# Performance work log

Hardware: AMD Instinct MI355X
Metric: run time of the kernel (lower is better)

## Reference

```python
import jax, jax.numpy as jnp
import numpy as np

B, S, D, MAXOBJ = 512, 77, 2048, 4
EPS = 1e-5


def _layer_norm(x, g, b):
    mu = jnp.mean(x, axis=-1, keepdims=True)
    var = jnp.mean((x - mu) ** 2, axis=-1, keepdims=True)
    return (x - mu) / jnp.sqrt(var + EPS) * g + b


def _mlp(x, ln_g, ln_b, w1, b1, w2, b2, residual):
    h = _layer_norm(x, ln_g, ln_b)
    h = jax.nn.gelu(h @ w1 + b1, approximate=False)
    h = h @ w2 + b2
    return h + x if residual else h


def setup_inputs() -> dict:
    key = jax.random.key(0)
    ks = jax.random.split(key, 8)
    sc = 0.02
    inputs_embeds = jax.random.normal(ks[0], (B, S, D), dtype=jnp.float32)
    # exactly one image token per sample -> mask sum matches fused rows
    pos = jax.random.randint(ks[1], (B,), 0, S)
    image_token_mask = (jnp.arange(S)[None, :] == pos[:, None])  # bool [B,S]
    object_embeds = jax.random.normal(ks[2], (B, MAXOBJ, 1, D), dtype=jnp.float32)
    num_objects = jax.random.randint(ks[3], (B,), 1, MAXOBJ + 1)  # >=1 objects
    return {
        "inputs_embeds": inputs_embeds,
        "object_embeds": object_embeds,
        "mlp1_ln_g": jnp.ones((2 * D,), jnp.float32),
        "mlp1_ln_b": jnp.zeros((2 * D,), jnp.float32),
        "mlp1_w1": sc * jax.random.normal(ks[4], (2 * D, D), jnp.float32),
        "mlp1_b1": jnp.zeros((D,), jnp.float32),
        "mlp1_w2": sc * jax.random.normal(ks[5], (D, D), jnp.float32),
        "mlp1_b2": jnp.zeros((D,), jnp.float32),
        "mlp2_ln_g": jnp.ones((D,), jnp.float32),
        "mlp2_ln_b": jnp.zeros((D,), jnp.float32),
        "mlp2_w1": sc * jax.random.normal(ks[6], (D, D), jnp.float32),
        "mlp2_b1": jnp.zeros((D,), jnp.float32),
        "mlp2_w2": sc * jax.random.normal(ks[7], (D, D), jnp.float32),
        "mlp2_b2": jnp.zeros((D,), jnp.float32),
        "ln_g": jnp.ones((D,), jnp.float32),
        "ln_b": jnp.zeros((D,), jnp.float32),
        "image_token_mask": image_token_mask,
        "num_objects": num_objects,
    }


def reference(inputs_embeds, object_embeds,
              mlp1_ln_g, mlp1_ln_b, mlp1_w1, mlp1_b1, mlp1_w2, mlp1_b2,
              mlp2_ln_g, mlp2_ln_b, mlp2_w1, mlp2_b1, mlp2_w2, mlp2_b2,
              ln_g, ln_b, image_token_mask, num_objects):
    b, s, d = inputs_embeds.shape
    max_obj = object_embeds.shape[1]
    dt = inputs_embeds.dtype
    # mean over valid objects per sample (fuse_object_embeddings ragged split+mean)
    valid = (jnp.arange(max_obj)[None, :] < num_objects[:, None]).astype(dt)  # [B,MAXOBJ]
    obj = object_embeds[:, :, 0, :]  # [B,MAXOBJ,D] (T==1 token per object)
    mean_obj = jnp.sum(obj * valid[:, :, None], axis=1) / num_objects[:, None].astype(dt)
    # gather the single image-token embed per row (mask has exactly one True per row)
    idx = jnp.argmax(image_token_mask, axis=1)  # [B]
    rows = jnp.arange(b)
    tok = inputs_embeds[rows, idx]  # [B,D]
    # fuse_fn: cat -> MLP1 (no residual) + tok -> MLP2 (residual) -> LayerNorm
    x = jnp.concatenate([tok, mean_obj], axis=-1)  # [B,2D]
    h = _mlp(x, mlp1_ln_g, mlp1_ln_b, mlp1_w1, mlp1_b1, mlp1_w2, mlp1_b2, residual=False) + tok
    h = _mlp(h, mlp2_ln_g, mlp2_ln_b, mlp2_w1, mlp2_b1, mlp2_w2, mlp2_b2, residual=True)
    h = _layer_norm(h, ln_g, ln_b)
    # masked_scatter_ back into the sequence
    out = inputs_embeds.at[rows, idx].set(h.astype(dt))
    return out
```

## Files before the change

kernel.cpp:

```cpp
#include <hip/hip_runtime.h>
#include <math.h>

#define B_ 512
#define S_ 77
#define D_ 2048
#define EPS_ 1e-5f

typedef __attribute__((ext_vector_type(8))) short bf16x8;
typedef __attribute__((ext_vector_type(4))) float f32x4;

__device__ __forceinline__ unsigned short f2bf(float f) {
  union { float f; unsigned u; } x; x.f = f;
  return (unsigned short)((x.u + 0x7FFFu + ((x.u >> 16) & 1u)) >> 16);
}

__device__ __forceinline__ void blockReduce2(float& a, float& b, float* sbuf) {
  #pragma unroll
  for (int off = 32; off > 0; off >>= 1) {
    a += __shfl_down(a, off, 64);
    b += __shfl_down(b, off, 64);
  }
  int lane = threadIdx.x & 63, wid = threadIdx.x >> 6;
  if (lane == 0) { sbuf[wid * 2] = a; sbuf[wid * 2 + 1] = b; }
  __syncthreads();
  if (threadIdx.x == 0) {
    float sa = 0.f, sb = 0.f;
    #pragma unroll
    for (int w = 0; w < 4; w++) { sa += sbuf[w * 2]; sb += sbuf[w * 2 + 1]; }
    sbuf[8] = sa; sbuf[9] = sb;
  }
  __syncthreads();
  a = sbuf[8]; b = sbuf[9];
}

__global__ __launch_bounds__(256)
void prep_wcvt_kernel(const float* __restrict__ w1, const float* __restrict__ w2,
                      const float* __restrict__ w3, const float* __restrict__ w4,
                      unsigned short* __restrict__ o1, unsigned short* __restrict__ o2,
                      unsigned short* __restrict__ o3, unsigned short* __restrict__ o4,
                      const float* __restrict__ x_embed, const float* __restrict__ obj,
                      const int* __restrict__ mask, const int* __restrict__ nobj,
                      const float* __restrict__ g, const float* __restrict__ bb,
                      int* __restrict__ idx_out, float* __restrict__ tok_out,
                      unsigned short* __restrict__ xln_out) {
  __shared__ unsigned short T[64 * 72];
  __shared__ int s_idx;
  __shared__ float sbuf[10];
  const int z = blockIdx.z;
  const int t = threadIdx.x;

  if (z == 4) {
    const int b = blockIdx.y * gridDim.x + blockIdx.x;
    if (b >= B_) return;
    if (t == 0) s_idx = 0;
    __syncthreads();
    for (int j = t; j < S_; j += 256)
      if (mask[b * S_ + j] != 0) atomicMax(&s_idx, j);
    __syncthreads();
    const int idx = s_idx;
    if (t == 0) idx_out[b] = idx;

    const float4* tokrow = (const float4*)(x_embed + ((long)b * S_ + idx) * D_);
    float4 t0 = tokrow[t * 2];
    float4 t1 = tokrow[t * 2 + 1];
    ((float4*)(tok_out + (long)b * D_))[t * 2] = t0;
    ((float4*)(tok_out + (long)b * D_))[t * 2 + 1] = t1;

    const int n = nobj[b];
    const float inv_n = 1.0f / (float)n;
    float4 s0 = make_float4(0.f, 0.f, 0.f, 0.f), s1 = s0;
    for (int o = 0; o < n; o++) {
      const float4* orow = (const float4*)(obj + ((long)b * 4 + o) * D_);
      float4 q0 = orow[t * 2], q1 = orow[t * 2 + 1];
      s0.x += q0.x; s0.y += q0.y; s0.z += q0.z; s0.w += q0.w;
      s1.x += q1.x; s1.y += q1.y; s1.z += q1.z; s1.w += q1.w;
    }
    float vals[16] = { t0.x, t0.y, t0.z, t0.w, t1.x, t1.y, t1.z, t1.w,
                       s0.x * inv_n, s0.y * inv_n, s0.z * inv_n, s0.w * inv_n,
                       s1.x * inv_n, s1.y * inv_n, s1.z * inv_n, s1.w * inv_n };
    float sum = 0.f, sq = 0.f;
    #pragma unroll
    for (int i = 0; i < 16; i++) { sum += vals[i]; sq += vals[i] * vals[i]; }
    blockReduce2(sum, sq, sbuf);
    const float mu = sum * (1.f / 4096.f);
    const float rstd = rsqrtf(sq * (1.f / 4096.f) - mu * mu + EPS_);
    #pragma unroll
    for (int i = 0; i < 16; i++) {
      int d = (i < 8) ? (t * 8 + i) : (D_ + t * 8 + (i - 8));
      float v = (vals[i] - mu) * rstd * g[d] + bb[d];
      xln_out[(long)b * (2 * D_) + d] = f2bf(v);
    }
    return;
  }

  const int K = (z == 0) ? 4096 : 2048;
  if ((int)blockIdx.y * 64 >= K) return;
  const float* W = (z == 0) ? w1 : (z == 1) ? w2 : (z == 2) ? w3 : w4;
  unsigned short* O = (z == 0) ? o1 : (z == 1) ? o2 : (z == 2) ? o3 : o4;
  const int k0 = blockIdx.y * 64, n0 = blockIdx.x * 64;
  const int r = t >> 4, c4 = (t & 15) * 4;
  #pragma unroll
  for (int rr = 0; rr < 4; rr++) {
    const int k = rr * 16 + r;
    float4 v = *(const float4*)&W[(long)(k0 + k) * 2048 + n0 + c4];
    T[(c4 + 0) * 72 + k] = f2bf(v.x);
    T[(c4 + 1) * 72 + k] = f2bf(v.y);
    T[(c4 + 2) * 72 + k] = f2bf(v.z);
    T[(c4 + 3) * 72 + k] = f2bf(v.w);
  }
  __syncthreads();
  const int n = t >> 3, k8 = (t & 7) * 8;
  *(uint4*)&O[(long)(n0 + n) * K + k0 + k8]      = *(const uint4*)&T[n * 72 + k8];
  *(uint4*)&O[(long)(n0 + n + 32) * K + k0 + k8] = *(const uint4*)&T[(n + 32) * 72 + k8];
}

template<int GELU, int HAS_RES, int OUT_BF16>
__global__ __launch_bounds__(256)
void gemm_kernel(const unsigned short* __restrict__ A, const unsigned short* __restrict__ Wt,
                 const float* __restrict__ bias, const float* __restrict__ res,
                 void* __restrict__ outp, int M, int N, int K,
                 const float4* __restrict__ csrc, float4* __restrict__ cdst, long cn4) {
  const int mblocks = M >> 6;
  if ((int)blockIdx.y >= mblocks) {
    const int cby = gridDim.y - mblocks;
    const long tcount = (long)cby * gridDim.x * blockDim.x;
    long i = ((long)((int)blockIdx.y - mblocks) * gridDim.x + blockIdx.x) * blockDim.x + threadIdx.x;
    const long lim = cn4 - 3 * tcount;
    for (; i < lim; i += 4 * tcount) {
      float4 v0 = csrc[i];
      float4 v1 = csrc[i + tcount];
      float4 v2 = csrc[i + 2 * tcount];
      float4 v3 = csrc[i + 3 * tcount];
      cdst[i] = v0;
      cdst[i + tcount] = v1;
      cdst[i + 2 * tcount] = v2;
      cdst[i + 3 * tcount] = v3;
    }
    for (; i < cn4; i += tcount) cdst[i] = csrc[i];
    return;
  }
  constexpr int LDA = 72;
  __shared__ __align__(16) unsigned short As[2][64 * LDA];
  __shared__ __align__(16) unsigned short Bs[2][64 * LDA];
  const int tid = threadIdx.x;
  const int m0 = blockIdx.y * 64;
  const int n0 = blockIdx.x * 64;
  const int lane = tid & 63;
  const int wave = tid >> 6;
  const int l16 = lane & 15;
  const int quad = lane >> 4;
  const int wm = (wave & 1) * 32;
  const int wn = (wave >> 1) * 32;
  const int srow = tid >> 3;
  const int scol = (tid & 7) * 8;

  const unsigned short* Ar0 = A  + (long)(m0 + srow) * K + scol;
  const unsigned short* Ar1 = A  + (long)(m0 + srow + 32) * K + scol;
  const unsigned short* Br0 = Wt + (long)(n0 + srow) * K + scol;
  const unsigned short* Br1 = Wt + (long)(n0 + srow + 32) * K + scol;

  f32x4 acc[2][2];
  #pragma unroll
  for (int i = 0; i < 2; i++)
    #pragma unroll
    for (int j = 0; j < 2; j++) acc[i][j] = (f32x4){0.f, 0.f, 0.f, 0.f};

  const int ntile = K >> 6;

  uint4 ra0 = *(const uint4*)Ar0, ra1 = *(const uint4*)Ar1;
  uint4 rb0 = *(const uint4*)Br0, rb1 = *(const uint4*)Br1;
  *(uint4*)&As[0][srow * LDA + scol]        = ra0;
  *(uint4*)&As[0][(srow + 32) * LDA + scol] = ra1;
  *(uint4*)&Bs[0][srow * LDA + scol]        = rb0;
  *(uint4*)&Bs[0][(srow + 32) * LDA + scol] = rb1;
  if (ntile > 1) {
    ra0 = *(const uint4*)(Ar0 + 64); ra1 = *(const uint4*)(Ar1 + 64);
    rb0 = *(const uint4*)(Br0 + 64); rb1 = *(const uint4*)(Br1 + 64);
  }
  __syncthreads();

  for (int t = 0; t < ntile; ++t) {
    const unsigned short* as = As[t & 1];
    const unsigned short* bs = Bs[t & 1];
    bf16x8 af[2][2], bg[2][2];
    #pragma unroll
    for (int kk = 0; kk < 2; kk++) {
      af[kk][0] = *(const bf16x8*)&as[(wm + l16) * LDA + kk * 32 + quad * 8];
      af[kk][1] = *(const bf16x8*)&as[(wm + 16 + l16) * LDA + kk * 32 + quad * 8];
      bg[kk][0] = *(const bf16x8*)&bs[(wn + l16) * LDA + kk * 32 + quad * 8];
      bg[kk][1] = *(const bf16x8*)&bs[(wn + 16 + l16) * LDA + kk * 32 + quad * 8];
    }
    if (t + 1 < ntile) {
      unsigned short* an = As[(t + 1) & 1];
      unsigned short* bn = Bs[(t + 1) & 1];
      *(uint4*)&an[srow * LDA + scol]        = ra0;
      *(uint4*)&an[(srow + 32) * LDA + scol] = ra1;
      *(uint4*)&bn[srow * LDA + scol]        = rb0;
      *(uint4*)&bn[(srow + 32) * LDA + scol] = rb1;
      if (t + 2 < ntile) {
        const int off = (t + 2) << 6;
        ra0 = *(const uint4*)(Ar0 + off); ra1 = *(const uint4*)(Ar1 + off);
        rb0 = *(const uint4*)(Br0 + off); rb1 = *(const uint4*)(Br1 + off);
      }
    }
    #pragma unroll
    for (int kk = 0; kk < 2; kk++)
      #pragma unroll
      for (int mt = 0; mt < 2; mt++)
        #pragma unroll
        for (int nt2 = 0; nt2 < 2; nt2++)
          acc[mt][nt2] = __builtin_amdgcn_mfma_f32_16x16x32_bf16(af[kk][mt], bg[kk][nt2], acc[mt][nt2], 0, 0, 0);
    __syncthreads();
  }
  #pragma unroll
  for (int mt = 0; mt < 2; mt++) {
    #pragma unroll
    for (int nt2 = 0; nt2 < 2; nt2++) {
      const int col = n0 + wn + nt2 * 16 + l16;
      const float bc = bias[col];
      #pragma unroll
      for (int r = 0; r < 4; r++) {
        const int row = m0 + wm + mt * 16 + quad * 4 + r;
        float v = acc[mt][nt2][r] + bc;
        if constexpr (HAS_RES) v += res[(long)row * N + col];
        if constexpr (GELU) v = 0.5f * v * (1.f + erff(v * 0.70710678118654752f));
        if constexpr (OUT_BF16)
          ((unsigned short*)outp)[(long)row * N + col] = f2bf(v);
        else
          ((float*)outp)[(long)row * N + col] = v;
      }
    }
  }
}

__global__ __launch_bounds__(256)
void ln_bf16_kernel(const float* __restrict__ in, const float* __restrict__ g,
                    const float* __restrict__ bb, unsigned short* __restrict__ out) {
  __shared__ float sbuf[10];
  const int b = blockIdx.x, t = threadIdx.x;
  const float4* row = (const float4*)(in + (long)b * D_);
  float4 v0 = row[t * 2], v1 = row[t * 2 + 1];
  float o[8] = { v0.x, v0.y, v0.z, v0.w, v1.x, v1.y, v1.z, v1.w };
  float sum = 0.f, sq = 0.f;
  #pragma unroll
  for (int i = 0; i < 8; i++) { sum += o[i]; sq += o[i] * o[i]; }
  blockReduce2(sum, sq, sbuf);
  const float mu = sum * (1.f / 2048.f);
  const float rstd = rsqrtf(sq * (1.f / 2048.f) - mu * mu + EPS_);
  const int d0 = t * 8;
  #pragma unroll
  for (int i = 0; i < 8; i++)
    out[(long)b * D_ + d0 + i] = f2bf((o[i] - mu) * rstd * g[d0 + i] + bb[d0 + i]);
}

__global__ __launch_bounds__(256)
void final_kernel(const float* __restrict__ in, const float* __restrict__ g,
                  const float* __restrict__ bb, const int* __restrict__ idxbuf,
                  float* __restrict__ out) {
  __shared__ float sbuf[10];
  const int b = blockIdx.x, t = threadIdx.x;
  const float4* row = (const float4*)(in + (long)b * D_);
  float4 v0 = row[t * 2], v1 = row[t * 2 + 1];
  float o[8] = { v0.x, v0.y, v0.z, v0.w, v1.x, v1.y, v1.z, v1.w };
  float sum = 0.f, sq = 0.f;
  #pragma unroll
  for (int i = 0; i < 8; i++) { sum += o[i]; sq += o[i] * o[i]; }
  blockReduce2(sum, sq, sbuf);
  const float mu = sum * (1.f / 2048.f);
  const float rstd = rsqrtf(sq * (1.f / 2048.f) - mu * mu + EPS_);
  float* orow = out + ((long)b * S_ + idxbuf[b]) * D_;
  const int d0 = t * 8;
  #pragma unroll
  for (int i = 0; i < 8; i++) o[i] = (o[i] - mu) * rstd * g[d0 + i] + bb[d0 + i];
  ((float4*)orow)[t * 2]     = make_float4(o[0], o[1], o[2], o[3]);
  ((float4*)orow)[t * 2 + 1] = make_float4(o[4], o[5], o[6], o[7]);
}

extern "C" void kernel_launch(void* const* d_in, const int* in_sizes, int n_in,
                              void* d_out, int out_size, void* d_ws, size_t ws_size,
                              hipStream_t stream) {
  const float* inputs_embeds = (const float*)d_in[0];
  const float* object_embeds = (const float*)d_in[1];
  const float* mlp1_ln_g = (const float*)d_in[2];
  const float* mlp1_ln_b = (const float*)d_in[3];
  const float* mlp1_w1   = (const float*)d_in[4];
  const float* mlp1_b1   = (const float*)d_in[5];
  const float* mlp1_w2   = (const float*)d_in[6];
  const float* mlp1_b2   = (const float*)d_in[7];
  const float* mlp2_ln_g = (const float*)d_in[8];
  const float* mlp2_ln_b = (const float*)d_in[9];
  const float* mlp2_w1   = (const float*)d_in[10];
  const float* mlp2_b1   = (const float*)d_in[11];
  const float* mlp2_w2   = (const float*)d_in[12];
  const float* mlp2_b2   = (const float*)d_in[13];
  const float* ln_g      = (const float*)d_in[14];
  const float* ln_b      = (const float*)d_in[15];
  const int* mask        = (const int*)d_in[16];
  const int* nobj        = (const int*)d_in[17];

  char* ws = (char*)d_ws;
  int*            idxbuf = (int*)ws;
  float*          tok    = (float*)(ws + 4096);
  unsigned short* xln    = (unsigned short*)(ws + 4096 + 4194304);
  unsigned short* h1     = (unsigned short*)(ws + 4096 + 8388608);
  float*          h2     = (float*)(ws + 4096 + 10485760);
  unsigned short* x2ln   = (unsigned short*)(ws + 4096 + 14680064);
  unsigned short* h3     = (unsigned short*)(ws + 4096 + 16777216);
  float*          h4     = (float*)(ws + 4096 + 18874368);
  char*           wbase  = ws + 4096 + 18874368 + 4194304;
  unsigned short* w1t    = (unsigned short*)(wbase);
  unsigned short* w2t    = (unsigned short*)(wbase + 16777216);
  unsigned short* w3t    = (unsigned short*)(wbase + 25165824);
  unsigned short* w4t    = (unsigned short*)(wbase + 33554432);

  prep_wcvt_kernel<<<dim3(32, 64, 5), 256, 0, stream>>>(
      mlp1_w1, mlp1_w2, mlp2_w1, mlp2_w2, w1t, w2t, w3t, w4t,
      inputs_embeds, object_embeds, mask, nobj, mlp1_ln_g, mlp1_ln_b,
      idxbuf, tok, xln);

  const float4* in4 = (const float4*)inputs_embeds;
  float4* out4 = (float4*)d_out;
  const long n4 = (long)B_ * S_ * D_ / 4;
  const long ch = n4 / 4;

  dim3 gg(2048 / 64, B_ / 64 + 16);
  gemm_kernel<1, 0, 1><<<gg, 256, 0, stream>>>(xln,  w1t, mlp1_b1, nullptr, h1, B_, D_, 2 * D_,
                                               in4 + 0 * ch, out4 + 0 * ch, ch);
  gemm_kernel<0, 1, 0><<<gg, 256, 0, stream>>>(h1,   w2t, mlp1_b2, tok,     h2, B_, D_, D_,
                                               in4 + 1 * ch, out4 + 1 * ch, ch);
  ln_bf16_kernel<<<B_, 256, 0, stream>>>(h2, mlp2_ln_g, mlp2_ln_b, x2ln);
  gemm_kernel<1, 0, 1><<<gg, 256, 0, stream>>>(x2ln, w3t, mlp2_b1, nullptr, h3, B_, D_, D_,
                                               in4 + 2 * ch, out4 + 2 * ch, ch);
  gemm_kernel<0, 1, 0><<<gg, 256, 0, stream>>>(h3,   w4t, mlp2_b2, h2,      h4, B_, D_, D_,
                                               in4 + 3 * ch, out4 + 3 * ch, ch);
  final_kernel<<<B_, 256, 0, stream>>>(h4, ln_g, ln_b, idxbuf, (float*)d_out);
}
```

Baseline: 680.9 us.

## Move embed copy into prep kernel and deepen GEMM global-load prefetch to four stages

The full inputs_embeds to output copy no longer rides in extra blocks of each of the four GEMM launches. It now runs as a sixth z-slice of the weight-conversion/prep kernel, so the GEMMs launch only their compute tiles. The GEMM main loop is unrolled by four with register staging that issues global loads four K-tiles ahead, while keeping double-buffered LDS. This hides more memory latency but raises register pressure, and the copy now competes with weight conversion instead of overlapping the GEMMs.

```diff
diff --git a/kernel.cpp b/kernel.cpp
--- a/kernel.cpp
+++ b/kernel.cpp
@@ -34,20 +34,38 @@
 }
 
 __global__ __launch_bounds__(256)
-void prep_wcvt_kernel(const float* __restrict__ w1, const float* __restrict__ w2,
-                      const float* __restrict__ w3, const float* __restrict__ w4,
-                      unsigned short* __restrict__ o1, unsigned short* __restrict__ o2,
-                      unsigned short* __restrict__ o3, unsigned short* __restrict__ o4,
-                      const float* __restrict__ x_embed, const float* __restrict__ obj,
-                      const int* __restrict__ mask, const int* __restrict__ nobj,
-                      const float* __restrict__ g, const float* __restrict__ bb,
-                      int* __restrict__ idx_out, float* __restrict__ tok_out,
-                      unsigned short* __restrict__ xln_out) {
+void mega_stream_kernel(const float* __restrict__ w1, const float* __restrict__ w2,
+                        const float* __restrict__ w3, const float* __restrict__ w4,
+                        unsigned short* __restrict__ o1, unsigned short* __restrict__ o2,
+                        unsigned short* __restrict__ o3, unsigned short* __restrict__ o4,
+                        const float* __restrict__ x_embed, const float* __restrict__ obj,
+                        const int* __restrict__ mask, const int* __restrict__ nobj,
+                        const float* __restrict__ g, const float* __restrict__ bb,
+                        int* __restrict__ idx_out, float* __restrict__ tok_out,
+                        unsigned short* __restrict__ xln_out,
+                        const float4* __restrict__ csrc, float4* __restrict__ cdst, long cn4) {
   __shared__ unsigned short T[64 * 72];
   __shared__ int s_idx;
   __shared__ float sbuf[10];
   const int z = blockIdx.z;
   const int t = threadIdx.x;
+
+  if (z == 5) {
+    const long tcount = (long)2048 * 256;
+    long i = ((long)blockIdx.y * gridDim.x + blockIdx.x) * 256 + t;
+    for (; i + 3 * tcount < cn4; i += 4 * tcount) {
+      float4 v0 = csrc[i];
+      float4 v1 = csrc[i + tcount];
+      float4 v2 = csrc[i + 2 * tcount];
+      float4 v3 = csrc[i + 3 * tcount];
+      cdst[i] = v0;
+      cdst[i + tcount] = v1;
+      cdst[i + 2 * tcount] = v2;
+      cdst[i + 3 * tcount] = v3;
+    }
+    for (; i < cn4; i += tcount) cdst[i] = csrc[i];
+    return;
+  }
 
   if (z == 4) {
     const int b = blockIdx.y * gridDim.x + blockIdx.x;
@@ -114,31 +132,46 @@
   *(uint4*)&O[(long)(n0 + n + 32) * K + k0 + k8] = *(const uint4*)&T[(n + 32) * 72 + k8];
 }
 
+
+#define DECL_STAGE(s) uint4 sa0_##s, sa1_##s, sb0_##s, sb1_##s;
+#define LOAD_STAGE(s, tt) { const long off_ = (long)(tt) << 6; \
+  sa0_##s = *(const uint4*)(Ar0 + off_); sa1_##s = *(const uint4*)(Ar1 + off_); \
+  sb0_##s = *(const uint4*)(Br0 + off_); sb1_##s = *(const uint4*)(Br1 + off_); }
+#define WRITE_STAGE(s, buf) { \
+  *(uint4*)&As[buf][srow * LDA + scol]        = sa0_##s; \
+  *(uint4*)&As[buf][(srow + 32) * LDA + scol] = sa1_##s; \
+  *(uint4*)&Bs[buf][srow * LDA + scol]        = sb0_##s; \
+  *(uint4*)&Bs[buf][(srow + 32) * LDA + scol] = sb1_##s; }
+
+#define GEMM_STEP(c, snext, curbuf, nextbuf) { \
+  const int t_ = tb + (c); \
+  if (t_ + 4 < ntile) LOAD_STAGE(c, t_ + 4) \
+  const unsigned short* as_ = As[curbuf]; \
+  const unsigned short* bs_ = Bs[curbuf]; \
+  bf16x8 af[2][2], bg[2][2]; \
+  _Pragma("unroll") \
+  for (int kk = 0; kk < 2; kk++) { \
+    af[kk][0] = *(const bf16x8*)&as_[(wm + l16) * LDA + kk * 32 + quad * 8]; \
+    af[kk][1] = *(const bf16x8*)&as_[(wm + 16 + l16) * LDA + kk * 32 + quad * 8]; \
+    bg[kk][0] = *(const bf16x8*)&bs_[(wn + l16) * LDA + kk * 32 + quad * 8]; \
+    bg[kk][1] = *(const bf16x8*)&bs_[(wn + 16 + l16) * LDA + kk * 32 + quad * 8]; \
+  } \
+  _Pragma("unroll") \
+  for (int kk = 0; kk < 2; kk++) \
+    _Pragma("unroll") \
+    for (int mt = 0; mt < 2; mt++) \
+      _Pragma("unroll") \
+      for (int nt2 = 0; nt2 < 2; nt2++) \
+        acc[mt][nt2] = __builtin_amdgcn_mfma_f32_16x16x32_bf16(af[kk][mt], bg[kk][nt2], acc[mt][nt2], 0, 0, 0); \
+  if (t_ + 1 < ntile) WRITE_STAGE(snext, nextbuf) \
+  __syncthreads(); \
+}
+
 template<int GELU, int HAS_RES, int OUT_BF16>
 __global__ __launch_bounds__(256)
 void gemm_kernel(const unsigned short* __restrict__ A, const unsigned short* __restrict__ Wt,
                  const float* __restrict__ bias, const float* __restrict__ res,
-                 void* __restrict__ outp, int M, int N, int K,
-                 const float4* __restrict__ csrc, float4* __restrict__ cdst, long cn4) {
-  const int mblocks = M >> 6;
-  if ((int)blockIdx.y >= mblocks) {
-    const int cby = gridDim.y - mblocks;
-    const long tcount = (long)cby * gridDim.x * blockDim.x;
-    long i = ((long)((int)blockIdx.y - mblocks) * gridDim.x + blockIdx.x) * blockDim.x + threadIdx.x;
-    const long lim = cn4 - 3 * tcount;
-    for (; i < lim; i += 4 * tcount) {
-      float4 v0 = csrc[i];
-      float4 v1 = csrc[i + tcount];
-      float4 v2 = csrc[i + 2 * tcount];
-      float4 v3 = csrc[i + 3 * tcount];
-      cdst[i] = v0;
-      cdst[i + tcount] = v1;
-      cdst[i + 2 * tcount] = v2;
-      cdst[i + 3 * tcount] = v3;
-    }
-    for (; i < cn4; i += tcount) cdst[i] = csrc[i];
-    return;
-  }
+                 void* __restrict__ outp, int M, int N, int K) {
   constexpr int LDA = 72;
   __shared__ __align__(16) unsigned short As[2][64 * LDA];
   __shared__ __align__(16) unsigned short Bs[2][64 * LDA];
@@ -167,51 +200,18 @@
 
   const int ntile = K >> 6;
 
-  uint4 ra0 = *(const uint4*)Ar0, ra1 = *(const uint4*)Ar1;
-  uint4 rb0 = *(const uint4*)Br0, rb1 = *(const uint4*)Br1;
-  *(uint4*)&As[0][srow * LDA + scol]        = ra0;
-  *(uint4*)&As[0][(srow + 32) * LDA + scol] = ra1;
-  *(uint4*)&Bs[0][srow * LDA + scol]        = rb0;
-  *(uint4*)&Bs[0][(srow + 32) * LDA + scol] = rb1;
-  if (ntile > 1) {
-    ra0 = *(const uint4*)(Ar0 + 64); ra1 = *(const uint4*)(Ar1 + 64);
-    rb0 = *(const uint4*)(Br0 + 64); rb1 = *(const uint4*)(Br1 + 64);
-  }
+  DECL_STAGE(0) DECL_STAGE(1) DECL_STAGE(2) DECL_STAGE(3)
+  LOAD_STAGE(0, 0) LOAD_STAGE(1, 1) LOAD_STAGE(2, 2) LOAD_STAGE(3, 3)
+  WRITE_STAGE(0, 0)
   __syncthreads();
 
-  for (int t = 0; t < ntile; ++t) {
-    const unsigned short* as = As[t & 1];
-    const unsigned short* bs = Bs[t & 1];
-    bf16x8 af[2][2], bg[2][2];
-    #pragma unroll
-    for (int kk = 0; kk < 2; kk++) {
-      af[kk][0] = *(const bf16x8*)&as[(wm + l16) * LDA + kk * 32 + quad * 8];
-      af[kk][1] = *(const bf16x8*)&as[(wm + 16 + l16) * LDA + kk * 32 + quad * 8];
-      bg[kk][0] = *(const bf16x8*)&bs[(wn + l16) * LDA + kk * 32 + quad * 8];
-      bg[kk][1] = *(const bf16x8*)&bs[(wn + 16 + l16) * LDA + kk * 32 + quad * 8];
-    }
-    if (t + 1 < ntile) {
-      unsigned short* an = As[(t + 1) & 1];
-      unsigned short* bn = Bs[(t + 1) & 1];
-      *(uint4*)&an[srow * LDA + scol]        = ra0;
-      *(uint4*)&an[(srow + 32) * LDA + scol] = ra1;
-      *(uint4*)&bn[srow * LDA + scol]        = rb0;
-      *(uint4*)&bn[(srow + 32) * LDA + scol] = rb1;
-      if (t + 2 < ntile) {
-        const int off = (t + 2) << 6;
-        ra0 = *(const uint4*)(Ar0 + off); ra1 = *(const uint4*)(Ar1 + off);
-        rb0 = *(const uint4*)(Br0 + off); rb1 = *(const uint4*)(Br1 + off);
-      }
-    }
-    #pragma unroll
-    for (int kk = 0; kk < 2; kk++)
-      #pragma unroll
-      for (int mt = 0; mt < 2; mt++)
-        #pragma unroll
-        for (int nt2 = 0; nt2 < 2; nt2++)
-          acc[mt][nt2] = __builtin_amdgcn_mfma_f32_16x16x32_bf16(af[kk][mt], bg[kk][nt2], acc[mt][nt2], 0, 0, 0);
-    __syncthreads();
-  }
+  for (int tb = 0; tb < ntile; tb += 4) {
+    GEMM_STEP(0, 1, 0, 1)
+    GEMM_STEP(1, 2, 1, 0)
+    GEMM_STEP(2, 3, 0, 1)
+    GEMM_STEP(3, 0, 1, 0)
+  }
+
   #pragma unroll
   for (int mt = 0; mt < 2; mt++) {
     #pragma unroll
@@ -313,25 +313,19 @@
   unsigned short* w3t    = (unsigned short*)(wbase + 25165824);
   unsigned short* w4t    = (unsigned short*)(wbase + 33554432);
 
-  prep_wcvt_kernel<<<dim3(32, 64, 5), 256, 0, stream>>>(
+  const long n4 = (long)B_ * S_ * D_ / 4;
+
+  mega_stream_kernel<<<dim3(32, 64, 6), 256, 0, stream>>>(
       mlp1_w1, mlp1_w2, mlp2_w1, mlp2_w2, w1t, w2t, w3t, w4t,
       inputs_embeds, object_embeds, mask, nobj, mlp1_ln_g, mlp1_ln_b,
-      idxbuf, tok, xln);
-
-  const float4* in4 = (const float4*)inputs_embeds;
-  float4* out4 = (float4*)d_out;
-  const long n4 = (long)B_ * S_ * D_ / 4;
-  const long ch = n4 / 4;
-
-  dim3 gg(2048 / 64, B_ / 64 + 16);
-  gemm_kernel<1, 0, 1><<<gg, 256, 0, stream>>>(xln,  w1t, mlp1_b1, nullptr, h1, B_, D_, 2 * D_,
-                                               in4 + 0 * ch, out4 + 0 * ch, ch);
-  gemm_kernel<0, 1, 0><<<gg, 256, 0, stream>>>(h1,   w2t, mlp1_b2, tok,     h2, B_, D_, D_,
-                                               in4 + 1 * ch, out4 + 1 * ch, ch);
+      idxbuf, tok, xln,
+      (const float4*)inputs_embeds, (float4*)d_out, n4);
+
+  dim3 gg(2048 / 64, B_ / 64);
+  gemm_kernel<1, 0, 1><<<gg, 256, 0, stream>>>(xln,  w1t, mlp1_b1, nullptr, h1, B_, D_, 2 * D_);
+  gemm_kernel<0, 1, 0><<<gg, 256, 0, stream>>>(h1,   w2t, mlp1_b2, tok,     h2, B_, D_, D_);
   ln_bf16_kernel<<<B_, 256, 0, stream>>>(h2, mlp2_ln_g, mlp2_ln_b, x2ln);
-  gemm_kernel<1, 0, 1><<<gg, 256, 0, stream>>>(x2ln, w3t, mlp2_b1, nullptr, h3, B_, D_, D_,
-                                               in4 + 2 * ch, out4 + 2 * ch, ch);
-  gemm_kernel<0, 1, 0><<<gg, 256, 0, stream>>>(h3,   w4t, mlp2_b2, h2,      h4, B_, D_, D_,
-                                               in4 + 3 * ch, out4 + 3 * ch, ch);
+  gemm_kernel<1, 0, 1><<<gg, 256, 0, stream>>>(x2ln, w3t, mlp2_b1, nullptr, h3, B_, D_, D_);
+  gemm_kernel<0, 1, 0><<<gg, 256, 0, stream>>>(h3,   w4t, mlp2_b2, h2,      h4, B_, D_, D_);
   final_kernel<<<B_, 256, 0, stream>>>(h4, ln_g, ln_b, idxbuf, (float*)d_out);
 }
```

Result: slower. 762.2 us (+11.9%).
